# Kernel optimization log

Hardware: AMD Instinct MI355X
Metric: run time of the kernel (lower is better)

## Reference

```python
import jax, jax.numpy as jnp
import numpy as np


def _tconv(x, w, b):
    # x: [B,C_in,N,T], w: [C_out,C_in,1,k] -> 'same' padding along T only
    pad = (w.shape[-1] - 1) // 2
    y = jax.lax.conv_general_dilated(x, w, (1, 1), [(0, 0), (pad, pad)],
                                     dimension_numbers=('NCHW', 'OIHW', 'NCHW'))
    return y + b[None, :, None, None]


def _temporal(x, w1, b1, w2, b2, w3, b3):
    # x: [B,T,N,C] -> gated GLU-style temporal conv -> [B,T,N,C_out]
    xc = jnp.transpose(x, (0, 3, 2, 1))  # [B,C,N,T]
    p = _tconv(xc, w1, b1)
    q = jax.nn.sigmoid(_tconv(xc, w2, b2))
    h = jax.nn.relu(p * q + _tconv(xc, w3, b3))
    return jnp.transpose(h, (0, 3, 2, 1))


def _cheb(x, src, dst, wn, W, bias):
    # x: [M,N,C]; scaled Laplacian with lambda_max=2 => L_hat = -D^-1/2 A D^-1/2
    # (diag +1 from L and -1 self-loop fill cancel exactly, as in PyG ChebConv)
    N = x.shape[1]

    def spmv(v):
        msgs = v[:, src, :] * wn[None, :, None]
        return jnp.zeros_like(v).at[:, dst, :].add(msgs)

    Tx0 = x
    out = jnp.einsum('mnc,cd->mnd', Tx0, W[0])
    Tx1 = spmv(Tx0)
    out = out + jnp.einsum('mnc,cd->mnd', Tx1, W[1])
    Txp, Txpp = Tx1, Tx0
    for k in range(2, W.shape[0]):
        Txk = 2.0 * spmv(Txp) - Txpp
        out = out + jnp.einsum('mnc,cd->mnd', Txk, W[k])
        Txpp, Txp = Txp, Txk
    return out + bias


def _bn_train(out, gamma, beta, eps=1e-5):
    # BatchNorm2d in training mode (batch stats, biased variance) over [B,C,N,T]
    ob = jnp.transpose(out, (0, 3, 2, 1))
    mu = jnp.mean(ob, axis=(0, 2, 3), keepdims=True)
    var = jnp.mean((ob - mu) ** 2, axis=(0, 2, 3), keepdims=True)
    ob = (ob - mu) * jax.lax.rsqrt(var + eps)
    ob = ob * gamma[None, :, None, None] + beta[None, :, None, None]
    return jnp.transpose(ob, (0, 3, 2, 1))


def setup_inputs():
    B, T, N, Cin, H, k, K, E = 16, 12, 4096, 2, 64, 3, 3, 65536
    ks = jax.random.split(jax.random.key(0), 20)
    sc = 0.1
    return {
        'x': jax.random.normal(ks[0], (B, T, N, Cin), jnp.float32),
        'edge_index': jax.random.randint(ks[1], (2, E), 0, N),
        'edge_attr': jax.random.uniform(ks[2], (E,), jnp.float32),
        't1_w1': jax.random.normal(ks[3], (H, Cin, 1, k), jnp.float32) * sc,
        't1_b1': jnp.zeros((H,), jnp.float32),
        't1_w2': jax.random.normal(ks[4], (H, Cin, 1, k), jnp.float32) * sc,
        't1_b2': jnp.zeros((H,), jnp.float32),
        't1_w3': jax.random.normal(ks[5], (H, Cin, 1, k), jnp.float32) * sc,
        't1_b3': jnp.zeros((H,), jnp.float32),
        'cheb_W': jax.random.normal(ks[6], (K, H, H), jnp.float32) * sc,
        'cheb_b': jnp.zeros((H,), jnp.float32),
        't2_w1': jax.random.normal(ks[7], (H, H, 1, k), jnp.float32) * sc,
        't2_b1': jnp.zeros((H,), jnp.float32),
        't2_w2': jax.random.normal(ks[8], (H, H, 1, k), jnp.float32) * sc,
        't2_b2': jnp.zeros((H,), jnp.float32),
        't2_w3': jax.random.normal(ks[9], (H, H, 1, k), jnp.float32) * sc,
        't2_b3': jnp.zeros((H,), jnp.float32),
        'bn_g': jnp.ones((H,), jnp.float32),
        'bn_b': jnp.zeros((H,), jnp.float32),
    }


def reference(x, edge_index, edge_attr,
              t1_w1, t1_b1, t1_w2, t1_b2, t1_w3, t1_b3,
              cheb_W, cheb_b,
              t2_w1, t2_b1, t2_w2, t2_b2, t2_w3, t2_b3,
              bn_g, bn_b):
    t1 = _temporal(x, t1_w1, t1_b1, t1_w2, t1_b2, t1_w3, t1_b3)  # [B,T,N,H]
    B, T, N, C = t1.shape
    src, dst = edge_index[0], edge_index[1]
    # sym normalization: deg from source scatter; -D^-1/2 w D^-1/2 edge weights
    deg = jnp.zeros((N,), t1.dtype).at[src].add(edge_attr)
    safe = jnp.where(deg > 0, deg, 1.0)
    dis = jnp.where(deg > 0, jax.lax.rsqrt(safe), 0.0)
    wn = -dis[src] * edge_attr * dis[dst]
    g = _cheb(t1.reshape(B * T, N, C), src, dst, wn, cheb_W, cheb_b)
    g = jax.nn.relu(g).reshape(B, T, N, C)
    out = _temporal(g, t2_w1, t2_b1, t2_w2, t2_b2, t2_w3, t2_b3)
    return _bn_train(out, bn_g, bn_b)
```

## Files before the change

### kernel.cpp

```cpp
#include <hip/hip_runtime.h>
#include <stdint.h>

#define BB 16
#define TT 12
#define NN 4096
#define HH 64
#define EE 65536
#define MM (BB*TT)
#define ROWS (MM*NN)
#define TOT (ROWS*HH)
#define NBUCKET 256

typedef __attribute__((ext_vector_type(8))) __bf16 bf16x8;
typedef __attribute__((ext_vector_type(8))) unsigned short us8;
typedef __attribute__((ext_vector_type(4))) float f32x4;

__device__ __forceinline__ unsigned short f2bf(float f){
  unsigned u = __builtin_bit_cast(unsigned, f);
  u += 0x7fffu + ((u >> 16) & 1u);
  return (unsigned short)(u >> 16);
}
__device__ __forceinline__ float bf2f(unsigned short s){
  unsigned u = ((unsigned)s) << 16;
  return __builtin_bit_cast(float, u);
}
__device__ __forceinline__ bf16x8 ldbf8(const unsigned short* p){
  us8 u = *reinterpret_cast<const us8*>(p);
  return __builtin_bit_cast(bf16x8, u);
}


__global__ void k_deg_cnt(const int* __restrict__ src, const int* __restrict__ dst,
                          const float* __restrict__ attr,
                          float* __restrict__ deg, int* __restrict__ cnt){
  int e = blockIdx.x * 256 + threadIdx.x;
  if (e < EE){
    atomicAdd(&deg[src[e]], attr[e]);
    atomicAdd(&cnt[dst[e]], 1);
  }
}

__global__ void k_wn(const int* __restrict__ src, const int* __restrict__ dst,
                     const float* __restrict__ attr, const float* __restrict__ deg,
                     float* __restrict__ wn){
  int e = blockIdx.x * 256 + threadIdx.x;
  if (e < EE){
    float ds = deg[src[e]], dd = deg[dst[e]];
    float rs = ds > 0.f ? rsqrtf(ds) : 0.f;
    float rd = dd > 0.f ? rsqrtf(dd) : 0.f;
    wn[e] = -rs * attr[e] * rd;
  }
}

__global__ void k_scan(const int* __restrict__ cnt, int* __restrict__ rowptr,
                       int* __restrict__ fill){
  __shared__ int lds[1024];
  int t = threadIdx.x;
  int c0 = cnt[4*t], c1 = cnt[4*t+1], c2 = cnt[4*t+2], c3 = cnt[4*t+3];
  int s = c0 + c1 + c2 + c3;
  lds[t] = s; __syncthreads();
  for (int off = 1; off < 1024; off <<= 1){
    int v = (t >= off) ? lds[t-off] : 0;
    __syncthreads();
    lds[t] += v;
    __syncthreads();
  }
  int excl = lds[t] - s;
  rowptr[4*t]   = excl;            fill[4*t]   = excl;
  rowptr[4*t+1] = excl + c0;       fill[4*t+1] = excl + c0;
  rowptr[4*t+2] = excl + c0 + c1;  fill[4*t+2] = excl + c0 + c1;
  rowptr[4*t+3] = excl + c0+c1+c2; fill[4*t+3] = excl + c0+c1+c2;
  if (t == 1023) rowptr[4096] = lds[1023];
}

__global__ void k_csr(const int* __restrict__ dst, const int* __restrict__ src,
                      const float* __restrict__ wn, int* __restrict__ fill,
                      int* __restrict__ csrs, float* __restrict__ csrw){
  int e = blockIdx.x * 256 + threadIdx.x;
  if (e < EE){
    int d = dst[e];
    int pos = atomicAdd(&fill[d], 1);
    csrs[pos] = src[e];
    csrw[pos] = wn[e];
  }
}


__global__ void k_wprep(const float* __restrict__ chebW,
                        const float* __restrict__ w1, const float* __restrict__ w2,
                        const float* __restrict__ w3,
                        const float* __restrict__ e1w, const float* __restrict__ e1b,
                        const float* __restrict__ e2w, const float* __restrict__ e2b,
                        const float* __restrict__ e3w, const float* __restrict__ e3b,
                        unsigned short* __restrict__ wfD, unsigned short* __restrict__ wfF,
                        unsigned short* __restrict__ wfE){
  int gt = blockIdx.x * blockDim.x + threadIdx.x;
  int stride = gridDim.x * blockDim.x;
  for (int i = gt; i < 12288; i += stride){
    int kl = i & 31, cc = (i >> 5) & 63, mk = i >> 11;
    int kt = mk & 1, mat = mk >> 1;
    int k = kt * 32 + kl;
    float v;
    if (mat == 0)      v = chebW[k*64 + cc] - chebW[2*4096 + k*64 + cc];
    else if (mat == 1) v = chebW[4096 + k*64 + cc];
    else               v = 2.f * chebW[2*4096 + k*64 + cc];
    wfD[i] = f2bf(v);
  }
  for (int i = gt; i < 36864; i += stride){
    int kl = i & 31, hh = (i >> 5) & 63, ck = i >> 11;
    int kt = ck % 6, conv = ck / 6;
    int k = kt * 32 + kl, dt = k >> 6, ci = k & 63;
    const float* w = (conv == 0) ? w1 : ((conv == 1) ? w2 : w3);
    wfF[i] = f2bf(w[(hh*64 + ci)*3 + dt]);
  }
  for (int i = gt; i < 6144; i += stride){
    int k = i & 31, hh = (i >> 5) & 63, conv = i >> 11;
    const float* w = (conv == 0) ? e1w : ((conv == 1) ? e2w : e3w);
    const float* b = (conv == 0) ? e1b : ((conv == 1) ? e2b : e3b);
    float v = 0.f;
    if (k < 6)       v = w[(hh*2 + (k & 1))*3 + (k >> 1)];
    else if (k == 6) v = b[hh];
    wfE[i] = f2bf(v);
  }
}


__global__ __launch_bounds__(256) void k_temporal1(
    const float* __restrict__ x, const unsigned short* __restrict__ wfE,
    unsigned short* __restrict__ U){
  const int tid = threadIdx.x;
  const int wv = tid >> 6, lane = tid & 63;
  const int lhi = lane >> 4, llo = lane & 15;
  const int blk = blockIdx.x;
  const int bt = blk >> 6, nb = blk & 63;
  const int t = bt - (bt / TT) * TT;

  us8 au = {0,0,0,0,0,0,0,0};
  if (lhi == 0){
    const int n = nb*64 + wv*16 + llo;
    #pragma unroll
    for (int dt = 0; dt < 3; ++dt){
      int tp = t + dt - 1;
      if (tp >= 0 && tp < TT){
        const float2 v = *reinterpret_cast<const float2*>(
            x + ((size_t)(bt + dt - 1) * NN + n) * 2);
        if (dt == 0){ au[0] = f2bf(v.x); au[1] = f2bf(v.y); }
        if (dt == 1){ au[2] = f2bf(v.x); au[3] = f2bf(v.y); }
        if (dt == 2){ au[4] = f2bf(v.x); au[5] = f2bf(v.y); }
      }
    }
    au[6] = 0x3f80;
  }
  const bf16x8 af = __builtin_bit_cast(bf16x8, au);

  const f32x4 z = {0.f, 0.f, 0.f, 0.f};
  f32x4 acc[3][4];
  #pragma unroll
  for (int conv = 0; conv < 3; ++conv)
    #pragma unroll
    for (int ht = 0; ht < 4; ++ht){
      bf16x8 bw = ldbf8(wfE + (size_t)((conv*64) + ht*16 + llo)*32 + lhi*8);
      acc[conv][ht] = __builtin_amdgcn_mfma_f32_16x16x32_bf16(af, bw, z, 0, 0, 0);
    }

  #pragma unroll
  for (int ht = 0; ht < 4; ++ht){
    const int h = ht*16 + llo;
    #pragma unroll
    for (int i = 0; i < 4; ++i){
      float p = acc[0][ht][i];
      float q = acc[1][ht][i];
      float r = acc[2][ht][i];
      float sig = 1.f / (1.f + __expf(-q));
      float o = fmaxf(fmaf(p, sig, r), 0.f);
      const int n = nb*64 + wv*16 + lhi*4 + i;
      U[((size_t)bt * NN + n) * 64 + h] = f2bf(o);
    }
  }
}


template<int PHASE>
__global__ __launch_bounds__(256) void k_spmv(
    const unsigned short* __restrict__ X,
    const int* __restrict__ rowptr,
    const int* __restrict__ csrs, const float* __restrict__ csrw,
    const unsigned short* __restrict__ G0bf,
    unsigned short* __restrict__ Y){
  constexpr int MT = 4;
  constexpr int EU = 8;
  const int nb = gridDim.x;
  int bs = (blockIdx.x & 7) * (nb >> 3) + (blockIdx.x >> 3);
  int wg = bs * 4 + (threadIdx.x >> 6);
  wg = __builtin_amdgcn_readfirstlane(wg);
  const int lane = threadIdx.x & 63;
  const int mg = wg >> 12, n = wg & (NN-1);
  int e0 = __builtin_amdgcn_readfirstlane(rowptr[n]);
  int e1 = __builtin_amdgcn_readfirstlane(rowptr[n+1]);
  const unsigned short* Xb = X + (((size_t)mg * MT) << 12) * 64 + lane;

  float acc[MT];
  #pragma unroll
  for (int j = 0; j < MT; ++j) acc[j] = 0.f;

  for (int e = e0; e < e1; e += EU){
    int ss[EU]; float ww[EU];
    #pragma unroll
    for (int u = 0; u < EU; ++u){
      int ee = e + u;
      bool in = ee < e1;
      ss[u] = csrs[in ? ee : e0];
      ww[u] = in ? csrw[ee] : 0.f;
    }
    unsigned short v[EU][MT];
    #pragma unroll
    for (int u = 0; u < EU; ++u){
      #pragma unroll
      for (int j = 0; j < MT; ++j)
        v[u][j] = Xb[j * (NN*64) + (ss[u] << 6)];
    }
    #pragma unroll
    for (int u = 0; u < EU; ++u)
      #pragma unroll
      for (int j = 0; j < MT; ++j)
        acc[j] = fmaf(ww[u], bf2f(v[u][j]), acc[j]);
  }

  #pragma unroll
  for (int j = 0; j < MT; ++j){
    size_t idx = (((size_t)(mg * MT + j) * NN) + n) * 64 + lane;
    if (PHASE == 1){
      Y[idx] = f2bf(acc[j]);
    } else {
      float gv = bf2f(G0bf[idx]) + acc[j];
      Y[idx] = f2bf(fmaxf(gv, 0.f));
    }
  }
}


__global__ __launch_bounds__(256) void k_cheb_gemm(
    const unsigned short* __restrict__ U, const unsigned short* __restrict__ V,
    const unsigned short* __restrict__ wfD, const float* __restrict__ cheb_b,
    unsigned short* __restrict__ G0bf, unsigned short* __restrict__ P){
  const int tid = threadIdx.x;
  const int wv = tid >> 6, lane = tid & 63;
  const int lhi = lane >> 4, llo = lane & 15;
  const int rbase = blockIdx.x * 64;
  const int c = wv * 16 + llo;

  bf16x8 bA[2], bW1[2], bW2[2];
  #pragma unroll
  for (int kt = 0; kt < 2; ++kt){
    bA[kt]  = ldbf8(wfD + (size_t)((0*2 + kt)*64 + c)*32 + lhi*8);
    bW1[kt] = ldbf8(wfD + (size_t)((1*2 + kt)*64 + c)*32 + lhi*8);
    bW2[kt] = ldbf8(wfD + (size_t)((2*2 + kt)*64 + c)*32 + lhi*8);
  }
  f32x4 z = {0.f, 0.f, 0.f, 0.f};
  f32x4 accG[4], accP[4];
  #pragma unroll
  for (int rt = 0; rt < 4; ++rt){ accG[rt] = z; accP[rt] = z; }

  #pragma unroll
  for (int rt = 0; rt < 4; ++rt){
    const size_t r = (size_t)rbase + rt*16 + llo;
    const unsigned short* up = U + r*64 + lhi*8;
    const unsigned short* vp = V + r*64 + lhi*8;
    #pragma unroll
    for (int kt = 0; kt < 2; ++kt){
      bf16x8 au = ldbf8(up + kt*32);
      bf16x8 av = ldbf8(vp + kt*32);
      accG[rt] = __builtin_amdgcn_mfma_f32_16x16x32_bf16(au, bA[kt],  accG[rt], 0, 0, 0);
      accG[rt] = __builtin_amdgcn_mfma_f32_16x16x32_bf16(av, bW1[kt], accG[rt], 0, 0, 0);
      accP[rt] = __builtin_amdgcn_mfma_f32_16x16x32_bf16(av, bW2[kt], accP[rt], 0, 0, 0);
    }
  }
  __syncthreads();
  float bias = cheb_b[c];
  #pragma unroll
  for (int rt = 0; rt < 4; ++rt){
    #pragma unroll
    for (int i = 0; i < 4; ++i){
      size_t row = (size_t)rbase + rt*16 + lhi*4 + i;
      G0bf[row*64 + c] = f2bf(accG[rt][i] + bias);
      P[row*64 + c]    = f2bf(accP[rt][i]);
    }
  }
}


__global__ __launch_bounds__(256, 4) void k_temporal2(
    const unsigned short* __restrict__ g,
    const unsigned short* __restrict__ wfF,
    const float* __restrict__ b1, const float* __restrict__ b2, const float* __restrict__ b3,
    unsigned short* __restrict__ obf, float* __restrict__ bnstat2){
  const int tid = threadIdx.x;
  const int wv = tid >> 6, lane = tid & 63;
  const int lhi = lane >> 4, llo = lane & 15;
  const int blk = blockIdx.x;
  const int bt = blk >> 6, nb = blk & 63;
  const int t = bt - (bt / TT) * TT;
  const int h = wv * 16 + llo;

  f32x4 z = {0.f, 0.f, 0.f, 0.f};
  f32x4 acc[3][4];
  #pragma unroll
  for (int cv = 0; cv < 3; ++cv)
    #pragma unroll
    for (int rt = 0; rt < 4; ++rt) acc[cv][rt] = z;

  #pragma unroll
  for (int kt = 0; kt < 6; ++kt){
    const int dt = kt >> 1;
    const int tp = t + dt - 1;
    const bool ok = (tp >= 0) && (tp < TT);
    bf16x8 w0 = ldbf8(wfF + (size_t)((0*6 + kt)*64 + h)*32 + lhi*8);
    bf16x8 w1 = ldbf8(wfF + (size_t)((1*6 + kt)*64 + h)*32 + lhi*8);
    bf16x8 w2 = ldbf8(wfF + (size_t)((2*6 + kt)*64 + h)*32 + lhi*8);
    const unsigned short* gb = g + ((size_t)(bt + dt - 1) * NN) * 64 + (kt & 1)*32 + lhi*8;
    #pragma unroll
    for (int rt = 0; rt < 4; ++rt){
      bf16x8 a{};
      if (ok){
        size_t r = (size_t)nb*64 + rt*16 + llo;
        a = ldbf8(gb + r*64);
      }
      acc[0][rt] = __builtin_amdgcn_mfma_f32_16x16x32_bf16(w0, a, acc[0][rt], 0, 0, 0);
      acc[1][rt] = __builtin_amdgcn_mfma_f32_16x16x32_bf16(w1, a, acc[1][rt], 0, 0, 0);
      acc[2][rt] = __builtin_amdgcn_mfma_f32_16x16x32_bf16(w2, a, acc[2][rt], 0, 0, 0);
    }
  }

  const int h0 = wv*16 + lhi*4;
  const f32x4 vb1 = *reinterpret_cast<const f32x4*>(b1 + h0);
  const f32x4 vb2 = *reinterpret_cast<const f32x4*>(b2 + h0);
  const f32x4 vb3 = *reinterpret_cast<const f32x4*>(b3 + h0);
  f32x4 lsum = z, lsq = z;
  #pragma unroll
  for (int rt = 0; rt < 4; ++rt){
    const int n = nb*64 + rt*16 + llo;
    ushort4 pk;
    unsigned short* pp = reinterpret_cast<unsigned short*>(&pk);
    #pragma unroll
    for (int i = 0; i < 4; ++i){
      float p = acc[0][rt][i] + vb1[i];
      float q = acc[1][rt][i] + vb2[i];
      float r = acc[2][rt][i] + vb3[i];
      float sig = 1.f / (1.f + __expf(-q));
      float o = fmaxf(fmaf(p, sig, r), 0.f);
      pp[i] = f2bf(o);
      lsum[i] += o; lsq[i] = fmaf(o, o, lsq[i]);
    }
    *reinterpret_cast<ushort4*>(&obf[((size_t)bt * NN + n) * 64 + h0]) = pk;
  }
  #pragma unroll
  for (int m = 1; m < 16; m <<= 1){
    #pragma unroll
    for (int i = 0; i < 4; ++i){
      lsum[i] += __shfl_xor(lsum[i], m);
      lsq[i]  += __shfl_xor(lsq[i], m);
    }
  }
  if (llo == 0){
    float* bs = bnstat2 + (size_t)(blk & (NBUCKET-1)) * 128;
    #pragma unroll
    for (int i = 0; i < 4; ++i){
      atomicAdd(&bs[h0 + i], lsum[i]);
      atomicAdd(&bs[64 + h0 + i], lsq[i]);
    }
  }
}


__global__ void k_bnfinal(const float* __restrict__ bnstat2, float* __restrict__ bnstat){
  int t = threadIdx.x;
  float s = 0.f;
  for (int b = 0; b < NBUCKET; ++b) s += bnstat2[(size_t)b * 128 + t];
  bnstat[t] = s;
}

__global__ __launch_bounds__(256) void k_bnapply(
    const unsigned short* __restrict__ obf, float* __restrict__ out,
    const float* __restrict__ bnstat,
    const float* __restrict__ gamma, const float* __restrict__ beta){
  __shared__ float ssc[64], sfb[64];
  int tid = threadIdx.x;
  if (tid < 64){
    const float inv = 1.f / (float)ROWS;
    float s = bnstat[tid], q = bnstat[64 + tid];
    float mu = s * inv;
    float var = q * inv - mu * mu;
    if (var < 0.f) var = 0.f;
    float sc = gamma[tid] * rsqrtf(var + 1e-5f);
    ssc[tid] = sc;
    sfb[tid] = beta[tid] - mu * sc;
  }
  __syncthreads();
  const int ngrp = TOT / 8;
  for (int i = blockIdx.x * 256 + tid; i < ngrp; i += gridDim.x * 256){
    us8 v = *reinterpret_cast<const us8*>(obf + (size_t)i * 8);
    const int c0 = (i * 8) & 63;
    f32x4 lo, hi;
    #pragma unroll
    for (int j = 0; j < 4; ++j)
      lo[j] = fmaf(bf2f(v[j]), ssc[c0 + j], sfb[c0 + j]);
    #pragma unroll
    for (int j = 0; j < 4; ++j)
      hi[j] = fmaf(bf2f(v[4 + j]), ssc[c0 + 4 + j], sfb[c0 + 4 + j]);
    *reinterpret_cast<f32x4*>(out + (size_t)i * 8)     = lo;
    *reinterpret_cast<f32x4*>(out + (size_t)i * 8 + 4) = hi;
  }
}


extern "C" void kernel_launch(void* const* d_in, const int* in_sizes, int n_in,
                              void* d_out, int out_size, void* d_ws, size_t ws_size,
                              hipStream_t stream){
  const float* x     = (const float*)d_in[0];
  const int*   ei    = (const int*)d_in[1];
  const float* attr  = (const float*)d_in[2];
  const float* t1w1  = (const float*)d_in[3];
  const float* t1b1  = (const float*)d_in[4];
  const float* t1w2  = (const float*)d_in[5];
  const float* t1b2  = (const float*)d_in[6];
  const float* t1w3  = (const float*)d_in[7];
  const float* t1b3  = (const float*)d_in[8];
  const float* chebW = (const float*)d_in[9];
  const float* chebB = (const float*)d_in[10];
  const float* t2w1  = (const float*)d_in[11];
  const float* t2b1  = (const float*)d_in[12];
  const float* t2w2  = (const float*)d_in[13];
  const float* t2b2  = (const float*)d_in[14];
  const float* t2w3  = (const float*)d_in[15];
  const float* t2b3  = (const float*)d_in[16];
  const float* bng   = (const float*)d_in[17];
  const float* bnb   = (const float*)d_in[18];
  const int* src = ei;
  const int* dst = ei + EE;

  const size_t SZ_U = (size_t)ROWS * 64 * 2;
  char* ws = (char*)d_ws;
  unsigned short* U = (unsigned short*)ws;
  unsigned short* V = (unsigned short*)(ws + SZ_U);
  size_t off = 2 * SZ_U;
  float* deg    = (float*)(ws + off); off += 4096 * 4;
  int*   cnt    = (int*)(ws + off);   off += 4096 * 4;
  int*   rowptr = (int*)(ws + off);   off += 4128 * 4;
  int*   fill   = (int*)(ws + off);   off += 4096 * 4;
  float* wn     = (float*)(ws + off); off += EE * 4;
  int*   csrs   = (int*)(ws + off);   off += EE * 4;
  float* csrw   = (float*)(ws + off); off += EE * 4;
  unsigned short* wfD = (unsigned short*)(ws + off); off += 12288 * 2;
  unsigned short* wfF = (unsigned short*)(ws + off); off += 36864 * 2;
  unsigned short* wfE = (unsigned short*)(ws + off); off += 6144 * 2;
  float* bnstat = (float*)(ws + off); off += 128 * 4;
  float* bnstat2 = (float*)(ws + off); off += NBUCKET * 128 * 4;

  unsigned short* G0bf = (unsigned short*)d_out;

  hipMemsetAsync(deg, 0, 4096 * 4, stream);
  hipMemsetAsync(cnt, 0, 4096 * 4, stream);
  hipMemsetAsync(bnstat2, 0, NBUCKET * 128 * 4, stream);

  k_deg_cnt<<<EE/256, 256, 0, stream>>>(src, dst, attr, deg, cnt);
  k_wn<<<EE/256, 256, 0, stream>>>(src, dst, attr, deg, wn);
  k_scan<<<1, 1024, 0, stream>>>(cnt, rowptr, fill);
  k_csr<<<EE/256, 256, 0, stream>>>(dst, src, wn, fill, csrs, csrw);
  k_wprep<<<64, 256, 0, stream>>>(chebW, t2w1, t2w2, t2w3,
                                  t1w1, t1b1, t1w2, t1b2, t1w3, t1b3,
                                  wfD, wfF, wfE);

  k_temporal1<<<ROWS/64, 256, 0, stream>>>(x, wfE, U);
  k_spmv<1><<<(MM/4)*NN/4, 256, 0, stream>>>(U, rowptr, csrs, csrw, (const unsigned short*)nullptr, V);
  k_cheb_gemm<<<ROWS/64, 256, 0, stream>>>(U, V, wfD, chebB, G0bf, U );
  k_spmv<2><<<(MM/4)*NN/4, 256, 0, stream>>>(U , rowptr, csrs, csrw, G0bf, V );
  k_temporal2<<<ROWS/64, 256, 0, stream>>>(V , wfF, t2b1, t2b2, t2b3, U , bnstat2);
  k_bnfinal<<<1, 128, 0, stream>>>(bnstat2, bnstat);
  k_bnapply<<<2048, 256, 0, stream>>>(U, (float*)d_out, bnstat, bng, bnb);
}
```

Measured before the change: 784.6 us.

## Make temporal2 a persistent kernel with double-buffered LDS tiles and register-resident weights

Turns k_temporal2 into a persistent kernel: a fixed grid of 2048 blocks, each walking 6 tiles. The next tile's three time-shifted input planes are prefetched into registers and then into an XOR-swizzled, double-buffered LDS buffer while the current tile runs its MFMAs. The gated-conv weights are loaded into registers once per block instead of once per tile. This is meant to hide global load latency and remove repeated weight loads. In exchange it uses 48KB of LDS per block, lowers launch bounds to 2 blocks per SIMD-group, adds a barrier per tile and raises register pressure.

Measured after the change: 678.0 us. -13.6%, faster.

```diff
diff --git a/kernel.cpp b/kernel.cpp
--- a/kernel.cpp
+++ b/kernel.cpp
@@ -10,6 +10,8 @@
 #define ROWS (MM*NN)
 #define TOT (ROWS*HH)
 #define NBUCKET 256
+#define T2_GRID 2048
+#define T2_NT 6
 
 typedef __attribute__((ext_vector_type(8))) __bf16 bf16x8;
 typedef __attribute__((ext_vector_type(8))) unsigned short us8;
@@ -289,84 +291,130 @@
 }
 
 
-__global__ __launch_bounds__(256, 4) void k_temporal2(
+__device__ __forceinline__ void t2_load(const unsigned short* __restrict__ g,
+                                        int tile, int tid, uint4* st){
+  const int bt = tile >> 6, nb = tile & 63;
+  const int t = bt - (bt / TT) * TT;
+  #pragma unroll
+  for (int j = 0; j < 6; ++j){
+    const int plane = j >> 1;
+    const int tp = t + plane - 1;
+    const int idx = ((j & 1) << 8) + tid;
+    const int row = idx >> 3;
+    const int innerb = (idx & 7) * 16;
+    if (tp >= 0 && tp < TT){
+      const unsigned short* sp = g
+          + ((size_t)(bt + plane - 1) * NN + nb*64 + row) * 64
+          + ((innerb ^ ((row & 7) << 4)) >> 1);
+      st[j] = *reinterpret_cast<const uint4*>(sp);
+    } else {
+      st[j] = make_uint4(0u, 0u, 0u, 0u);
+    }
+  }
+}
+
+__global__ __launch_bounds__(256, 2) void k_temporal2(
     const unsigned short* __restrict__ g,
     const unsigned short* __restrict__ wfF,
     const float* __restrict__ b1, const float* __restrict__ b2, const float* __restrict__ b3,
     unsigned short* __restrict__ obf, float* __restrict__ bnstat2){
+  __shared__ unsigned short smem[2][12288];
   const int tid = threadIdx.x;
   const int wv = tid >> 6, lane = tid & 63;
   const int lhi = lane >> 4, llo = lane & 15;
-  const int blk = blockIdx.x;
-  const int bt = blk >> 6, nb = blk & 63;
-  const int t = bt - (bt / TT) * TT;
   const int h = wv * 16 + llo;
-
-  f32x4 z = {0.f, 0.f, 0.f, 0.f};
-  f32x4 acc[3][4];
+  const int h0 = wv * 16 + lhi * 4;
+
+  bf16x8 bw[3][6];
   #pragma unroll
   for (int cv = 0; cv < 3; ++cv)
     #pragma unroll
-    for (int rt = 0; rt < 4; ++rt) acc[cv][rt] = z;
-
-  #pragma unroll
-  for (int kt = 0; kt < 6; ++kt){
-    const int dt = kt >> 1;
-    const int tp = t + dt - 1;
-    const bool ok = (tp >= 0) && (tp < TT);
-    bf16x8 w0 = ldbf8(wfF + (size_t)((0*6 + kt)*64 + h)*32 + lhi*8);
-    bf16x8 w1 = ldbf8(wfF + (size_t)((1*6 + kt)*64 + h)*32 + lhi*8);
-    bf16x8 w2 = ldbf8(wfF + (size_t)((2*6 + kt)*64 + h)*32 + lhi*8);
-    const unsigned short* gb = g + ((size_t)(bt + dt - 1) * NN) * 64 + (kt & 1)*32 + lhi*8;
-    #pragma unroll
-    for (int rt = 0; rt < 4; ++rt){
-      bf16x8 a{};
-      if (ok){
-        size_t r = (size_t)nb*64 + rt*16 + llo;
-        a = ldbf8(gb + r*64);
-      }
-      acc[0][rt] = __builtin_amdgcn_mfma_f32_16x16x32_bf16(w0, a, acc[0][rt], 0, 0, 0);
-      acc[1][rt] = __builtin_amdgcn_mfma_f32_16x16x32_bf16(w1, a, acc[1][rt], 0, 0, 0);
-      acc[2][rt] = __builtin_amdgcn_mfma_f32_16x16x32_bf16(w2, a, acc[2][rt], 0, 0, 0);
-    }
-  }
-
-  const int h0 = wv*16 + lhi*4;
+    for (int kt = 0; kt < 6; ++kt)
+      bw[cv][kt] = ldbf8(wfF + (size_t)((cv*6 + kt)*64 + h)*32 + lhi*8);
+
   const f32x4 vb1 = *reinterpret_cast<const f32x4*>(b1 + h0);
   const f32x4 vb2 = *reinterpret_cast<const f32x4*>(b2 + h0);
   const f32x4 vb3 = *reinterpret_cast<const f32x4*>(b3 + h0);
-  f32x4 lsum = z, lsq = z;
-  #pragma unroll
-  for (int rt = 0; rt < 4; ++rt){
-    const int n = nb*64 + rt*16 + llo;
-    ushort4 pk;
-    unsigned short* pp = reinterpret_cast<unsigned short*>(&pk);
-    #pragma unroll
-    for (int i = 0; i < 4; ++i){
-      float p = acc[0][rt][i] + vb1[i];
-      float q = acc[1][rt][i] + vb2[i];
-      float r = acc[2][rt][i] + vb3[i];
-      float sig = 1.f / (1.f + __expf(-q));
-      float o = fmaxf(fmaf(p, sig, r), 0.f);
-      pp[i] = f2bf(o);
-      lsum[i] += o; lsq[i] = fmaf(o, o, lsq[i]);
-    }
-    *reinterpret_cast<ushort4*>(&obf[((size_t)bt * NN + n) * 64 + h0]) = pk;
-  }
-  #pragma unroll
-  for (int m = 1; m < 16; m <<= 1){
-    #pragma unroll
-    for (int i = 0; i < 4; ++i){
-      lsum[i] += __shfl_xor(lsum[i], m);
-      lsq[i]  += __shfl_xor(lsq[i], m);
-    }
-  }
-  if (llo == 0){
-    float* bs = bnstat2 + (size_t)(blk & (NBUCKET-1)) * 128;
-    #pragma unroll
-    for (int i = 0; i < 4; ++i){
-      atomicAdd(&bs[h0 + i], lsum[i]);
-      atomicAdd(&bs[64 + h0 + i], lsq[i]);
+  const f32x4 z = {0.f, 0.f, 0.f, 0.f};
+
+  uint4 st[6];
+  t2_load(g, blockIdx.x, tid, st);
+  #pragma unroll
+  for (int j = 0; j < 6; ++j)
+    *reinterpret_cast<uint4*>(&smem[0][(size_t)(j*256 + tid) * 8]) = st[j];
+  __syncthreads();
+
+  int cur = 0;
+  for (int it = 0; it < T2_NT; ++it){
+    const int tile = blockIdx.x + it * T2_GRID;
+    const int bt = tile >> 6, nb = tile & 63;
+
+    if (it + 1 < T2_NT)
+      t2_load(g, tile + T2_GRID, tid, st);
+
+    const unsigned short* sb = smem[cur];
+    f32x4 acc[3][4];
+    #pragma unroll
+    for (int cv = 0; cv < 3; ++cv)
+      #pragma unroll
+      for (int rt = 0; rt < 4; ++rt) acc[cv][rt] = z;
+
+    #pragma unroll
+    for (int kt = 0; kt < 6; ++kt){
+      const int dt = kt >> 1;
+      const int qb = (kt & 1) * 64 + lhi * 16;
+      #pragma unroll
+      for (int rt = 0; rt < 4; ++rt){
+        const int row = rt*16 + llo;
+        bf16x8 a = __builtin_bit_cast(bf16x8, *reinterpret_cast<const us8*>(
+            sb + dt*4096 + row*64 + ((qb ^ ((row & 7) << 4)) >> 1)));
+        acc[0][rt] = __builtin_amdgcn_mfma_f32_16x16x32_bf16(bw[0][kt], a, acc[0][rt], 0, 0, 0);
+        acc[1][rt] = __builtin_amdgcn_mfma_f32_16x16x32_bf16(bw[1][kt], a, acc[1][rt], 0, 0, 0);
+        acc[2][rt] = __builtin_amdgcn_mfma_f32_16x16x32_bf16(bw[2][kt], a, acc[2][rt], 0, 0, 0);
+      }
+    }
+
+    f32x4 lsum = z, lsq = z;
+    #pragma unroll
+    for (int rt = 0; rt < 4; ++rt){
+      const int n = nb*64 + rt*16 + llo;
+      ushort4 pk;
+      unsigned short* pp = reinterpret_cast<unsigned short*>(&pk);
+      #pragma unroll
+      for (int i = 0; i < 4; ++i){
+        float p = acc[0][rt][i] + vb1[i];
+        float q = acc[1][rt][i] + vb2[i];
+        float r = acc[2][rt][i] + vb3[i];
+        float sig = 1.f / (1.f + __expf(-q));
+        float o = fmaxf(fmaf(p, sig, r), 0.f);
+        pp[i] = f2bf(o);
+        lsum[i] += o; lsq[i] = fmaf(o, o, lsq[i]);
+      }
+      *reinterpret_cast<ushort4*>(&obf[((size_t)bt * NN + n) * 64 + h0]) = pk;
+    }
+    #pragma unroll
+    for (int m = 1; m < 16; m <<= 1){
+      #pragma unroll
+      for (int i = 0; i < 4; ++i){
+        lsum[i] += __shfl_xor(lsum[i], m);
+        lsq[i]  += __shfl_xor(lsq[i], m);
+      }
+    }
+    if (llo == 0){
+      float* bs = bnstat2 + (size_t)(tile & (NBUCKET-1)) * 128;
+      #pragma unroll
+      for (int i = 0; i < 4; ++i){
+        atomicAdd(&bs[h0 + i], lsum[i]);
+        atomicAdd(&bs[64 + h0 + i], lsq[i]);
+      }
+    }
+
+    if (it + 1 < T2_NT){
+      #pragma unroll
+      for (int j = 0; j < 6; ++j)
+        *reinterpret_cast<uint4*>(&smem[cur ^ 1][(size_t)(j*256 + tid) * 8]) = st[j];
+      __syncthreads();
+      cur ^= 1;
     }
   }
 }
@@ -474,7 +522,7 @@
   k_spmv<1><<<(MM/4)*NN/4, 256, 0, stream>>>(U, rowptr, csrs, csrw, (const unsigned short*)nullptr, V);
   k_cheb_gemm<<<ROWS/64, 256, 0, stream>>>(U, V, wfD, chebB, G0bf, U );
   k_spmv<2><<<(MM/4)*NN/4, 256, 0, stream>>>(U , rowptr, csrs, csrw, G0bf, V );
-  k_temporal2<<<ROWS/64, 256, 0, stream>>>(V , wfF, t2b1, t2b2, t2b3, U , bnstat2);
+  k_temporal2<<<T2_GRID, 256, 0, stream>>>(V , wfF, t2b1, t2b2, t2b3, U , bnstat2);
   k_bnfinal<<<1, 128, 0, stream>>>(bnstat2, bnstat);
   k_bnapply<<<2048, 256, 0, stream>>>(U, (float*)d_out, bnstat, bng, bnb);
 }
```
